# Performance work log

Measured on AMD Instinct MI355X. Metric: run time of the kernel, lower is better.

Reference implementation:

```python
import jax, jax.numpy as jnp
import numpy as np

N_HEAD = 32
N_KV_HEAD = 8
HEAD_DIM = 64
ROPE_THETA = 10000.0


def apply_rope(x):
    # x: [B, H, T, D], interleaved-pair RoPE (rotary_embedding_torch style)
    B, H, T, D = x.shape
    inv_freq = 1.0 / (ROPE_THETA ** (jnp.arange(0, D, 2, dtype=jnp.float32) / D))  # [D/2]
    ang = jnp.arange(T, dtype=jnp.float32)[:, None] * inv_freq[None, :]  # [T, D/2]
    cos = jnp.cos(ang)[None, None].astype(x.dtype)  # [1,1,T,D/2]
    sin = jnp.sin(ang)[None, None].astype(x.dtype)
    xe = x[..., 0::2]
    xo = x[..., 1::2]
    re = xe * cos - xo * sin
    ro = xo * cos + xe * sin
    return jnp.stack([re, ro], axis=-1).reshape(B, H, T, D)


def setup_inputs() -> dict:
    key = jax.random.key(0)
    ks = jax.random.split(key, 5)
    B, T, C = 2, 2048, 2048
    kv_dim = N_KV_HEAD * HEAD_DIM
    s = 0.02
    return {
        "x": jax.random.normal(ks[0], (B, T, C), jnp.float32),
        "wq": jax.random.normal(ks[1], (C, C), jnp.float32) * s,
        "wk": jax.random.normal(ks[2], (C, kv_dim), jnp.float32) * s,
        "wv": jax.random.normal(ks[3], (C, kv_dim), jnp.float32) * s,
        "wo": jax.random.normal(ks[4], (C, C), jnp.float32) * s,
    }


def reference(x, wq, wk, wv, wo):
    B, T, C = x.shape
    hd = HEAD_DIM
    q = (x @ wq).reshape(B, T, N_HEAD, hd).transpose(0, 2, 1, 3)      # [B,H,T,d]
    k = (x @ wk).reshape(B, T, N_KV_HEAD, hd).transpose(0, 2, 1, 3)   # [B,Hkv,T,d]
    v = (x @ wv).reshape(B, T, N_KV_HEAD, hd).transpose(0, 2, 1, 3)
    q = apply_rope(q)
    k = apply_rope(k)
    rep = N_HEAD // N_KV_HEAD
    k = jnp.repeat(k, rep, axis=1)  # repeat_interleave over head dim
    v = jnp.repeat(v, rep, axis=1)
    att = jnp.einsum('bhqd,bhkd->bhqk', q, k) * (1.0 / np.sqrt(hd))
    causal = jnp.tril(jnp.ones((T, T), dtype=bool))
    att = jnp.where(causal[None, None], att, jnp.finfo(att.dtype).min)
    att = jax.nn.softmax(att, axis=-1)
    y = jnp.einsum('bhqk,bhkd->bhqd', att, v)
    y = y.transpose(0, 2, 1, 3).reshape(B, T, C)
    return y @ wo
```

## Files before the change

kernel.cpp:

```cpp
#include <hip/hip_runtime.h>
#include <hip/hip_bf16.h>
#include <cstdint>
#include <cstddef>


using bf16 = __hip_bfloat16;
using f32x4  = __attribute__((ext_vector_type(4))) float;
using f32x16 = __attribute__((ext_vector_type(16))) float;
using short8 = __attribute__((ext_vector_type(8))) short;
using u32x4  = __attribute__((ext_vector_type(4))) unsigned int;

typedef __attribute__((address_space(1))) const void* gp1_t;
typedef __attribute__((address_space(3))) void*       lp3_t;

#define GLOAD_LDS16(g, l)                                                     \
  __builtin_amdgcn_global_load_lds((gp1_t)(const void*)(g), (lp3_t)(void*)(l), 16, 0, 0)

#define MFMA32(a, b, c) __builtin_amdgcn_mfma_f32_32x32x16_bf16(a, b, c, 0, 0, 0)

static constexpr int Bd  = 2;
static constexpr int Td  = 2048;
static constexpr int Cd  = 2048;
static constexpr int NH  = 32;
static constexpr int NKV = 8;
static constexpr int HD  = 64;
static constexpr int Md  = Bd * Td;

__device__ inline float bf2f(unsigned short u) {
  union { unsigned int i; float f; } v; v.i = ((unsigned int)u) << 16; return v.f;
}
__device__ inline unsigned short f2bfbits(float f) {
  union { float f; unsigned int u; } v; v.f = f;
  unsigned int r = v.u + 0x7fffu + ((v.u >> 16) & 1u);
  return (unsigned short)(r >> 16);
}
__device__ inline unsigned int pkbf(float a, float b) {
  unsigned int r;
  asm("v_cvt_pk_bf16_f32 %0, %1, %2" : "=v"(r) : "v"(a), "v"(b));
  return r;
}
__device__ inline void plswapf(float& a, float& b) {
  asm("v_permlane32_swap_b32 %0, %1" : "+v"(a), "+v"(b));
}
__device__ inline void plswapu(unsigned int& a, unsigned int& b) {
  asm("v_permlane32_swap_b32 %0, %1" : "+v"(a), "+v"(b));
}
__device__ inline float hmax16(const f32x16& v) {
  float a0 = fmaxf(v[0], v[1]),   a1 = fmaxf(v[2], v[3]);
  float a2 = fmaxf(v[4], v[5]),   a3 = fmaxf(v[6], v[7]);
  float a4 = fmaxf(v[8], v[9]),   a5 = fmaxf(v[10], v[11]);
  float a6 = fmaxf(v[12], v[13]), a7 = fmaxf(v[14], v[15]);
  float b0 = fmaxf(a0, a1), b1 = fmaxf(a2, a3);
  float b2 = fmaxf(a4, a5), b3 = fmaxf(a6, a7);
  return fmaxf(fmaxf(b0, b1), fmaxf(b2, b3));
}
__device__ inline float hsum16(const f32x16& v) {
  float a0 = v[0]+v[1],   a1 = v[2]+v[3],   a2 = v[4]+v[5],   a3 = v[6]+v[7];
  float a4 = v[8]+v[9],   a5 = v[10]+v[11], a6 = v[12]+v[13], a7 = v[14]+v[15];
  float b0 = a0+a1, b1 = a2+a3, b2 = a4+a5, b3 = a6+a7;
  return (b0+b1)+(b2+b3);
}

__global__ __launch_bounds__(256) void prep1_kernel(const float* __restrict__ x,
                                                    const float* __restrict__ wq,
                                                    const float* __restrict__ wk,
                                                    const float* __restrict__ wv,
                                                    bf16* __restrict__ xb,
                                                    bf16* __restrict__ w1) {
  __shared__ float tile[32][33];
  int bid = blockIdx.x, tid = threadIdx.x;
  if (bid < 8192) {
    int i = bid * 256 + tid;
    float4 v = ((const float4*)x)[i];
    ushort4 o;
    o.x = f2bfbits(v.x); o.y = f2bfbits(v.y); o.z = f2bfbits(v.z); o.w = f2bfbits(v.w);
    ((ushort4*)xb)[i] = o;
    return;
  }
  const float* in; bf16* out; int Cc, bx, by;
  if (bid < 12288)      { int l = bid - 8192;  in = wq; out = w1;                        Cc = 2048; bx = l & 63; by = l >> 6; }
  else if (bid < 13312) { int l = bid - 12288; in = wk; out = w1 + (size_t)2048 * 2048;  Cc = 512;  bx = l & 15; by = l >> 4; }
  else                  { int l = bid - 13312; in = wv; out = w1 + (size_t)2560 * 2048;  Cc = 512;  bx = l & 15; by = l >> 4; }
  int tx = tid & 31, ty = tid >> 5;
  int col = bx * 32 + tx;
#pragma unroll
  for (int i = 0; i < 4; ++i) {
    int row = by * 32 + ty + i * 8;
    tile[ty + i * 8][tx] = in[(size_t)row * Cc + col];
  }
  __syncthreads();
#pragma unroll
  for (int i = 0; i < 4; ++i) {
    int orow = bx * 32 + ty + i * 8;
    int ocol = by * 32 + tx;
    out[(size_t)orow * 2048 + ocol] = __float2bfloat16(tile[tx][ty + i * 8]);
  }
}

__global__ __launch_bounds__(256) void prep2_kernel(const float* __restrict__ wo,
                                                    bf16* __restrict__ w1,
                                                    bf16* __restrict__ Q,
                                                    bf16* __restrict__ K,
                                                    int qpairs, int total) {
  __shared__ float tile[32][33];
  int bid = blockIdx.x, tid = threadIdx.x;
  if (bid < 4096) {
    int bx = bid & 63, by = bid >> 6;
    int tx = tid & 31, ty = tid >> 5;
    int col = bx * 32 + tx;
#pragma unroll
    for (int i = 0; i < 4; ++i) {
      int row = by * 32 + ty + i * 8;
      tile[ty + i * 8][tx] = wo[(size_t)row * 2048 + col];
    }
    __syncthreads();
#pragma unroll
    for (int i = 0; i < 4; ++i) {
      int orow = bx * 32 + ty + i * 8;
      int ocol = by * 32 + tx;
      w1[(size_t)orow * 2048 + ocol] = __float2bfloat16(tile[tx][ty + i * 8]);
    }
    return;
  }
  int i = (bid - 4096) * 256 + tid;
  if (i >= total) return;
  unsigned int* buf; int p; float sc;
  if (i < qpairs) { buf = (unsigned int*)Q; p = i; sc = 0.18033688011112042f; }
  else            { buf = (unsigned int*)K; p = i - qpairs; sc = 1.0f; }
  int d2 = p & 31;
  int t  = (p >> 5) & (Td - 1);
  unsigned int packed = buf[p];
  float xe = bf2f((unsigned short)(packed & 0xffffu));
  float xo = bf2f((unsigned short)(packed >> 16));
  float inv = __builtin_amdgcn_exp2f((float)d2 * (-13.287712379549449f / 32.0f));
  float ang = (float)t * inv;
  float rev = ang * 0.15915494309189535f;
  rev = rev - floorf(rev);
  float s = __builtin_amdgcn_sinf(rev);
  float c = __builtin_amdgcn_cosf(rev);
  float re = (xe * c - xo * s) * sc;
  float ro = (xo * c + xe * s) * sc;
  buf[p] = (unsigned int)f2bfbits(re) | ((unsigned int)f2bfbits(ro) << 16);
}

template <int MODE>
__global__ __launch_bounds__(256) void gemm_bf16(const bf16* __restrict__ A,
                                                 const bf16* __restrict__ Bt,
                                                 void* __restrict__ Cp,
                                                 int M, int N, int K) {
  __shared__ __align__(16) bf16 Al[128 * 64];
  __shared__ __align__(16) bf16 Bl[128 * 64];
  int tid = threadIdx.x;
  int w = tid >> 6, lane = tid & 63;
  int lr = lane & 15, lg = lane >> 4;
  int m0 = blockIdx.x * 128, n0 = blockIdx.y * 128;
  int wr = w >> 1, wc = w & 1;
  f32x4 acc[4][4] = {};

  size_t Kb = (size_t)K * 2;
  int c8 = lane & 7, r8 = lane >> 3;
  const char* Asrc = (const char*)A + (size_t)(m0 + w * 8 + r8) * Kb + ((c8 ^ r8) << 4);
  const char* Bsrc = (const char*)Bt + (size_t)(n0 + w * 8 + r8) * Kb + ((c8 ^ r8) << 4);
  char* Ald = (char*)Al + w * 1024;
  char* Bld = (char*)Bl + w * 1024;

  for (int kt = 0; kt < K; kt += 64) {
#pragma unroll
    for (int j = 0; j < 4; ++j) {
      GLOAD_LDS16(Asrc + (size_t)j * 32 * Kb + (size_t)kt * 2, Ald + j * 4096);
      GLOAD_LDS16(Bsrc + (size_t)j * 32 * Kb + (size_t)kt * 2, Bld + j * 4096);
    }
    __syncthreads();
#pragma unroll
    for (int kk = 0; kk < 2; ++kk) {
      short8 af[4], bfr[4];
#pragma unroll
      for (int f = 0; f < 4; ++f) {
        int ra = wr * 64 + f * 16 + lr;
        int rb = wc * 64 + f * 16 + lr;
        int cb = (((kk << 2) | lg) ^ (lr & 7)) << 4;
        af[f]  = *(const short8*)((const char*)Al + (size_t)ra * 128 + cb);
        bfr[f] = *(const short8*)((const char*)Bl + (size_t)rb * 128 + cb);
      }
#pragma unroll
      for (int i = 0; i < 4; ++i)
#pragma unroll
        for (int j = 0; j < 4; ++j)
          acc[i][j] = __builtin_amdgcn_mfma_f32_16x16x32_bf16(af[i], bfr[j], acc[i][j], 0, 0, 0);
    }
    __syncthreads();
  }

  bf16* Qb  = (bf16*)Cp;
  bf16* Kb2 = Qb + (size_t)Bd * NH * Td * HD;
  bf16* Vtb = Kb2 + (size_t)Bd * NKV * Td * HD;

  if (MODE == 3 && n0 >= 2560) {
    int h  = (n0 - 2560 + wc * 64) >> 6;
    int b  = m0 >> 11;
    int tg = (m0 & 2047) + wr * 64;
    char* tb = (w < 2 ? (char*)Al : (char*)Bl) + (w & 1) * 8192;
#pragma unroll
    for (int i = 0; i < 4; ++i)
#pragma unroll
      for (int j = 0; j < 4; ++j)
#pragma unroll
        for (int r = 0; r < 4; r += 2) {
          int d  = j * 16 + lr;
          int tt = i * 16 + lg * 4 + r;
          unsigned int pk = pkbf(acc[i][j][r], acc[i][j][r + 1]);
          *(unsigned int*)(tb + (((size_t)d * 128 + tt * 2) ^ ((d & 7) << 4))) = pk;
        }
    asm volatile("s_waitcnt lgkmcnt(0)" ::: "memory");
    __builtin_amdgcn_sched_barrier(0);
    char* Vdst = (char*)Vtb + ((((size_t)b * NKV + h) * 64) * Td + tg) * 2;
#pragma unroll
    for (int p = 0; p < 8; ++p) {
      int d  = p * 8 + (lane >> 3);
      int tc = lane & 7;
      u32x4 v = *(const u32x4*)(tb + (((size_t)d * 128 + tc * 16) ^ ((d & 7) << 4)));
      *(u32x4*)(Vdst + (size_t)d * Td * 2 + tc * 16) = v;
    }
    return;
  }

#pragma unroll
  for (int i = 0; i < 4; ++i) {
#pragma unroll
    for (int j = 0; j < 4; ++j) {
#pragma unroll
      for (int r = 0; r < 4; ++r) {
        int mrow = m0 + wr * 64 + i * 16 + lg * 4 + r;
        int ncol = n0 + wc * 64 + j * 16 + lr;
        float v = acc[i][j][r];
        if (MODE == 2) {
          ((float*)Cp)[(size_t)mrow * N + ncol] = v;
        } else {
          int b = mrow >> 11, t = mrow & 2047;
          if (n0 < 2048) {
            int h = ncol >> 6, d = ncol & 63;
            Qb[(((size_t)b * NH + h) * Td + t) * HD + d] = __float2bfloat16(v);
          } else {
            int cc = ncol - 2048;
            int h = cc >> 6, d = cc & 63;
            Kb2[(((size_t)b * NKV + h) * Td + t) * HD + d] = __float2bfloat16(v);
          }
        }
      }
    }
  }
}

__global__ __launch_bounds__(512, 4) void attn_kernel(const bf16* __restrict__ Q,
                                                      const bf16* __restrict__ K,
                                                      const bf16* __restrict__ Vt,
                                                      bf16* __restrict__ Y) {
  __shared__ __align__(16) char lds[2 * 16384];
  int tid = threadIdx.x, w = tid >> 6, lane = tid & 63;
  int lq = lane & 31;
  int H  = lane >> 5;
  int qb = 7 - (int)blockIdx.y;
  int bh = blockIdx.x;
  int b = bh >> 5, h = bh & 31, kvh = h >> 2;
  int q0w = qb * 256 + w * 32;
  int qg  = q0w + lq;
  int tmax = qb * 4 + (w >> 1);
  int Nt   = qb * 4 + 4;

  const bf16* Qp = Q + (((size_t)b * NH + h) * Td) * HD;
  const char* Kg = (const char*)(K + (((size_t)b * NKV + kvh) * Td) * HD);
  const char* Vg = (const char*)(Vt + (((size_t)b * NKV + kvh) * HD) * Td);

  short8 qf[4];
#pragma unroll
  for (int ck = 0; ck < 4; ++ck)
    qf[ck] = *(const short8*)(Qp + (size_t)qg * HD + ck * 16 + H * 8);

  int srow   = lane >> 3;
  int scol16 = ((lane & 7) ^ srow) << 4;
  const char* Ksrc0 = Kg + (size_t)(w * 8 + srow) * 128 + scol16;
  const char* Vsrc0 = Vg + (size_t)(w * 8 + srow) * 4096 + scol16;
  char* KldsW[2] = { lds + w * 1024,          lds + 16384 + w * 1024 };
  char* VldsW[2] = { lds + 8192 + w * 1024,   lds + 24576 + w * 1024 };

#define STAGE_KV(tt, bb) do {                                                 \
    GLOAD_LDS16(Ksrc0 + (size_t)(tt) * 64 * 128, KldsW[bb]);                  \
    GLOAD_LDS16(Vsrc0 + (size_t)(tt) * 128,      VldsW[bb]);                  \
  } while (0)

  f32x16 acc0 = {}, acc1 = {};
  float m = -3e38f, l = 0.0f;
  int swz = (lq & 7) << 4;
  int rb0 = lq * 128, rb1 = (32 + lq) * 128;

  STAGE_KV(0, 0);
  asm volatile("s_waitcnt vmcnt(0)" ::: "memory");
  __syncthreads();

  for (int t = 0; t < Nt; ++t) {
    int cur = t & 1;
    if (t + 1 < Nt) STAGE_KV(t + 1, cur ^ 1);
    if (t <= tmax) {
      const char* Kl = lds + cur * 16384;
      const char* Vl = Kl + 8192;
      f32x16 s0 = {}, s1 = {};
      __builtin_amdgcn_s_setprio(1);
#pragma unroll
      for (int ck = 0; ck < 4; ++ck) {
        int c = (H * 16 + ck * 32) ^ swz;
        short8 kf0 = *(const short8*)(Kl + rb0 + c);
        short8 kf1 = *(const short8*)(Kl + rb1 + c);
        s0 = MFMA32(kf0, qf[ck], s0);
        s1 = MFMA32(kf1, qf[ck], s1);
      }
      __builtin_amdgcn_s_setprio(0);
      if (t == tmax) {
        int kvb = t * 64;
#pragma unroll
        for (int rr = 0; rr < 16; ++rr) {
          int krel = (rr & 3) + 8 * (rr >> 2) + 4 * H;
          if (kvb + krel > qg)      s0[rr] = -3e38f;
          if (kvb + 32 + krel > qg) s1[rr] = -3e38f;
        }
      }
      float mx = fmaxf(hmax16(s0), hmax16(s1));
      {
        float mb = mx;
        asm("" : "+v"(mb));
        plswapf(mx, mb);
        mx = fmaxf(mx, mb);
      }
      if (__any(mx > m + 8.0f)) {
        float mn = fmaxf(m, mx);
        float al = __builtin_amdgcn_exp2f(m - mn);
        m = mn;
        l *= al;
#pragma unroll
        for (int rr = 0; rr < 16; ++rr) { acc0[rr] *= al; acc1[rr] *= al; }
      }
#pragma unroll
      for (int rr = 0; rr < 16; ++rr) {
        s0[rr] = __builtin_amdgcn_exp2f(s0[rr] - m);
        s1[rr] = __builtin_amdgcn_exp2f(s1[rr] - m);
      }
      float ps = hsum16(s0) + hsum16(s1);
      {
        float pb = ps;
        asm("" : "+v"(pb));
        plswapf(ps, pb);
        ps += pb;
      }
      l += ps;
      short8 pf[4];
#pragma unroll
      for (int tt = 0; tt < 2; ++tt) {
        const f32x16& sv = tt ? s1 : s0;
#pragma unroll
        for (int a2 = 0; a2 < 2; ++a2) {
          unsigned int A0 = pkbf(sv[8*a2 + 0], sv[8*a2 + 1]);
          unsigned int A1 = pkbf(sv[8*a2 + 2], sv[8*a2 + 3]);
          unsigned int B0 = pkbf(sv[8*a2 + 4], sv[8*a2 + 5]);
          unsigned int B1 = pkbf(sv[8*a2 + 6], sv[8*a2 + 7]);
          plswapu(A0, B0);
          plswapu(A1, B1);
          u32x4 t4;
          t4[0] = A0; t4[1] = A1; t4[2] = B0; t4[3] = B1;
          pf[2*tt + a2] = __builtin_bit_cast(short8, t4);
        }
      }
      __builtin_amdgcn_s_setprio(1);
#pragma unroll
      for (int ks = 0; ks < 4; ++ks) {
        int c = (H * 16 + ks * 32) ^ swz;
        short8 vf0 = *(const short8*)(Vl + rb0 + c);
        short8 vf1 = *(const short8*)(Vl + rb1 + c);
        acc0 = MFMA32(vf0, pf[ks], acc0);
        acc1 = MFMA32(vf1, pf[ks], acc1);
      }
      __builtin_amdgcn_s_setprio(0);
    }
    asm volatile("s_waitcnt vmcnt(0)" ::: "memory");
    __syncthreads();
  }
#undef STAGE_KV

  float rn = 1.0f / l;
  bf16* Yp = Y + ((size_t)b * Td + qg) * Cd + h * HD;
#pragma unroll
  for (int rr = 0; rr < 16; rr += 2) {
    int d = (rr & 3) + 8 * (rr >> 2) + 4 * H;
    unsigned int w0 = pkbf(acc0[rr] * rn, acc0[rr + 1] * rn);
    unsigned int w1 = pkbf(acc1[rr] * rn, acc1[rr + 1] * rn);
    *(unsigned int*)(Yp + d)      = w0;
    *(unsigned int*)(Yp + 32 + d) = w1;
  }
}

extern "C" void kernel_launch(void* const* d_in, const int* in_sizes, int n_in,
                              void* d_out, int out_size, void* d_ws, size_t ws_size,
                              hipStream_t stream) {
  const float* x  = (const float*)d_in[0];
  const float* wq = (const float*)d_in[1];
  const float* wk = (const float*)d_in[2];
  const float* wv = (const float*)d_in[3];
  const float* wo = (const float*)d_in[4];

  char* ws = (char*)d_ws;
  const size_t o_xb = 0;
  const size_t o_w1 = o_xb + (size_t)Md * Cd * 2;
  const size_t o_Q  = o_w1 + (size_t)3072 * Cd * 2;
  const size_t o_K  = o_Q + (size_t)Bd * NH * Td * HD * 2;
  const size_t o_V  = o_K + (size_t)Bd * NKV * Td * HD * 2;

  bf16* xb  = (bf16*)(ws + o_xb);
  bf16* w1  = (bf16*)(ws + o_w1);
  bf16* Qb  = (bf16*)(ws + o_Q);
  bf16* Kb  = (bf16*)(ws + o_K);
  bf16* Vtb = (bf16*)(ws + o_V);
  bf16* yb  = xb;

  prep1_kernel<<<dim3(14336), dim3(256), 0, stream>>>(x, wq, wk, wv, xb, w1);
  gemm_bf16<3><<<dim3(Md / 128, 3072 / 128), dim3(256), 0, stream>>>(xb, w1, Qb, Md, 3072, Cd);
  {
    int qpairs = Bd * NH * Td * HD / 2;
    int kpairs = Bd * NKV * Td * HD / 2;
    int total = qpairs + kpairs;
    prep2_kernel<<<dim3(4096 + 20480), dim3(256), 0, stream>>>(wo, w1, Qb, Kb, qpairs, total);
  }
  attn_kernel<<<dim3(Bd * NH, 8), dim3(512), 0, stream>>>(Qb, Kb, Vtb, yb);
  gemm_bf16<2><<<dim3(Md / 128, Cd / 128), dim3(256), 0, stream>>>(yb, w1, d_out, Md, Cd, Cd);
}
```

Before: 216.3 us.

## Fuse RoPE into QKV GEMM epilogue and double-buffer GEMM LDS tiles

Moves the RoPE rotation and Q scaling out of the separate prep2 pass into the QKV GEMM epilogue. The pair partner comes from a lane shuffle, and sin/cos are computed per element. This removes a full read-modify-write pass over Q and K, and prep2 becomes a plain wo transpose kernel. The GEMM also gets double-buffered LDS staging so the next K tile loads while the current one computes, with launch bounds set for 2 blocks per CU. The epilogue now does more transcendental work per output element, and the doubled LDS may limit occupancy.

```diff
diff --git a/kernel.cpp b/kernel.cpp
--- a/kernel.cpp
+++ b/kernel.cpp
@@ -97,59 +97,34 @@
   }
 }
 
-__global__ __launch_bounds__(256) void prep2_kernel(const float* __restrict__ wo,
-                                                    bf16* __restrict__ w1,
-                                                    bf16* __restrict__ Q,
-                                                    bf16* __restrict__ K,
-                                                    int qpairs, int total) {
+__global__ __launch_bounds__(256) void transpose_f2b(const float* __restrict__ in,
+                                                     bf16* __restrict__ out,
+                                                     int R, int Cc) {
   __shared__ float tile[32][33];
-  int bid = blockIdx.x, tid = threadIdx.x;
-  if (bid < 4096) {
-    int bx = bid & 63, by = bid >> 6;
-    int tx = tid & 31, ty = tid >> 5;
-    int col = bx * 32 + tx;
-#pragma unroll
-    for (int i = 0; i < 4; ++i) {
-      int row = by * 32 + ty + i * 8;
-      tile[ty + i * 8][tx] = wo[(size_t)row * 2048 + col];
-    }
-    __syncthreads();
-#pragma unroll
-    for (int i = 0; i < 4; ++i) {
-      int orow = bx * 32 + ty + i * 8;
-      int ocol = by * 32 + tx;
-      w1[(size_t)orow * 2048 + ocol] = __float2bfloat16(tile[tx][ty + i * 8]);
-    }
-    return;
-  }
-  int i = (bid - 4096) * 256 + tid;
-  if (i >= total) return;
-  unsigned int* buf; int p; float sc;
-  if (i < qpairs) { buf = (unsigned int*)Q; p = i; sc = 0.18033688011112042f; }
-  else            { buf = (unsigned int*)K; p = i - qpairs; sc = 1.0f; }
-  int d2 = p & 31;
-  int t  = (p >> 5) & (Td - 1);
-  unsigned int packed = buf[p];
-  float xe = bf2f((unsigned short)(packed & 0xffffu));
-  float xo = bf2f((unsigned short)(packed >> 16));
-  float inv = __builtin_amdgcn_exp2f((float)d2 * (-13.287712379549449f / 32.0f));
-  float ang = (float)t * inv;
-  float rev = ang * 0.15915494309189535f;
-  rev = rev - floorf(rev);
-  float s = __builtin_amdgcn_sinf(rev);
-  float c = __builtin_amdgcn_cosf(rev);
-  float re = (xe * c - xo * s) * sc;
-  float ro = (xo * c + xe * s) * sc;
-  buf[p] = (unsigned int)f2bfbits(re) | ((unsigned int)f2bfbits(ro) << 16);
+  int tx = threadIdx.x & 31, ty = threadIdx.x >> 5;
+  int bx = blockIdx.x, by = blockIdx.y;
+  int col = bx * 32 + tx;
+#pragma unroll
+  for (int i = 0; i < 4; ++i) {
+    int row = by * 32 + ty + i * 8;
+    tile[ty + i * 8][tx] = in[(size_t)row * Cc + col];
+  }
+  __syncthreads();
+#pragma unroll
+  for (int i = 0; i < 4; ++i) {
+    int orow = bx * 32 + ty + i * 8;
+    int ocol = by * 32 + tx;
+    out[(size_t)orow * R + ocol] = __float2bfloat16(tile[tx][ty + i * 8]);
+  }
 }
 
 template <int MODE>
-__global__ __launch_bounds__(256) void gemm_bf16(const bf16* __restrict__ A,
-                                                 const bf16* __restrict__ Bt,
-                                                 void* __restrict__ Cp,
-                                                 int M, int N, int K) {
-  __shared__ __align__(16) bf16 Al[128 * 64];
-  __shared__ __align__(16) bf16 Bl[128 * 64];
+__global__ __launch_bounds__(256, 2) void gemm_bf16(const bf16* __restrict__ A,
+                                                    const bf16* __restrict__ Bt,
+                                                    void* __restrict__ Cp,
+                                                    int M, int N, int K) {
+  __shared__ __align__(16) bf16 Al[2][128 * 64];
+  __shared__ __align__(16) bf16 Bl[2][128 * 64];
   int tid = threadIdx.x;
   int w = tid >> 6, lane = tid & 63;
   int lr = lane & 15, lg = lane >> 4;
@@ -161,16 +136,26 @@
   int c8 = lane & 7, r8 = lane >> 3;
   const char* Asrc = (const char*)A + (size_t)(m0 + w * 8 + r8) * Kb + ((c8 ^ r8) << 4);
   const char* Bsrc = (const char*)Bt + (size_t)(n0 + w * 8 + r8) * Kb + ((c8 ^ r8) << 4);
-  char* Ald = (char*)Al + w * 1024;
-  char* Bld = (char*)Bl + w * 1024;
-
-  for (int kt = 0; kt < K; kt += 64) {
-#pragma unroll
-    for (int j = 0; j < 4; ++j) {
-      GLOAD_LDS16(Asrc + (size_t)j * 32 * Kb + (size_t)kt * 2, Ald + j * 4096);
-      GLOAD_LDS16(Bsrc + (size_t)j * 32 * Kb + (size_t)kt * 2, Bld + j * 4096);
-    }
-    __syncthreads();
+
+#define GSTAGE(kt, bb) do {                                                   \
+    char* ald = (char*)&Al[bb][0] + w * 1024;                                 \
+    char* bld = (char*)&Bl[bb][0] + w * 1024;                                 \
+    _Pragma("unroll")                                                         \
+    for (int j = 0; j < 4; ++j) {                                             \
+      GLOAD_LDS16(Asrc + (size_t)j * 32 * Kb + (size_t)(kt) * 2, ald + j * 4096); \
+      GLOAD_LDS16(Bsrc + (size_t)j * 32 * Kb + (size_t)(kt) * 2, bld + j * 4096); \
+    }                                                                         \
+  } while (0)
+
+  int nkt = K >> 6;
+  GSTAGE(0, 0);
+  __syncthreads();
+
+  for (int t = 0; t < nkt; ++t) {
+    int cur = t & 1;
+    if (t + 1 < nkt) GSTAGE((t + 1) << 6, cur ^ 1);
+    const char* Ab = (const char*)&Al[cur][0];
+    const char* Bb = (const char*)&Bl[cur][0];
 #pragma unroll
     for (int kk = 0; kk < 2; ++kk) {
       short8 af[4], bfr[4];
@@ -179,8 +164,8 @@
         int ra = wr * 64 + f * 16 + lr;
         int rb = wc * 64 + f * 16 + lr;
         int cb = (((kk << 2) | lg) ^ (lr & 7)) << 4;
-        af[f]  = *(const short8*)((const char*)Al + (size_t)ra * 128 + cb);
-        bfr[f] = *(const short8*)((const char*)Bl + (size_t)rb * 128 + cb);
+        af[f]  = *(const short8*)(Ab + (size_t)ra * 128 + cb);
+        bfr[f] = *(const short8*)(Bb + (size_t)rb * 128 + cb);
       }
 #pragma unroll
       for (int i = 0; i < 4; ++i)
@@ -190,6 +175,7 @@
     }
     __syncthreads();
   }
+#undef GSTAGE
 
   bf16* Qb  = (bf16*)Cp;
   bf16* Kb2 = Qb + (size_t)Bd * NH * Td * HD;
@@ -199,7 +185,7 @@
     int h  = (n0 - 2560 + wc * 64) >> 6;
     int b  = m0 >> 11;
     int tg = (m0 & 2047) + wr * 64;
-    char* tb = (w < 2 ? (char*)Al : (char*)Bl) + (w & 1) * 8192;
+    char* tb = (w < 2 ? (char*)&Al[0][0] : (char*)&Bl[0][0]) + (w & 1) * 8192;
 #pragma unroll
     for (int i = 0; i < 4; ++i)
 #pragma unroll
@@ -224,31 +210,53 @@
     return;
   }
 
-#pragma unroll
-  for (int i = 0; i < 4; ++i) {
+  if (MODE == 3) {
+    const float RC = -0.41524101186092029f;
+    float sc = (n0 < 2048) ? 0.18033688011112042f : 1.0f;
+    int odd = lane & 1;
 #pragma unroll
     for (int j = 0; j < 4; ++j) {
+      int ncol = n0 + wc * 64 + j * 16 + lr;
+      int d  = ncol & 63;
+      float inv = __builtin_amdgcn_exp2f((float)(d >> 1) * RC);
+#pragma unroll
+      for (int i = 0; i < 4; ++i) {
+#pragma unroll
+        for (int r = 0; r < 4; ++r) {
+          int mrow = m0 + wr * 64 + i * 16 + lg * 4 + r;
+          int t = mrow & 2047;
+          float v = acc[i][j][r];
+          float p = __shfl_xor(v, 1);
+          float rev = (float)t * inv * 0.15915494309189535f;
+          rev = rev - floorf(rev);
+          float s = __builtin_amdgcn_sinf(rev);
+          float c = __builtin_amdgcn_cosf(rev);
+          float res = odd ? (v * c + p * s) : (v * c - p * s);
+          res *= sc;
+          int b = mrow >> 11;
+          if (n0 < 2048) {
+            int h = ncol >> 6;
+            Qb[(((size_t)b * NH + h) * Td + t) * HD + d] = __float2bfloat16(res);
+          } else {
+            int h = (ncol - 2048) >> 6;
+            Kb2[(((size_t)b * NKV + h) * Td + t) * HD + d] = __float2bfloat16(res);
+          }
+        }
+      }
+    }
+    return;
+  }
+
+#pragma unroll
+  for (int i = 0; i < 4; ++i)
+#pragma unroll
+    for (int j = 0; j < 4; ++j)
 #pragma unroll
       for (int r = 0; r < 4; ++r) {
         int mrow = m0 + wr * 64 + i * 16 + lg * 4 + r;
         int ncol = n0 + wc * 64 + j * 16 + lr;
-        float v = acc[i][j][r];
-        if (MODE == 2) {
-          ((float*)Cp)[(size_t)mrow * N + ncol] = v;
-        } else {
-          int b = mrow >> 11, t = mrow & 2047;
-          if (n0 < 2048) {
-            int h = ncol >> 6, d = ncol & 63;
-            Qb[(((size_t)b * NH + h) * Td + t) * HD + d] = __float2bfloat16(v);
-          } else {
-            int cc = ncol - 2048;
-            int h = cc >> 6, d = cc & 63;
-            Kb2[(((size_t)b * NKV + h) * Td + t) * HD + d] = __float2bfloat16(v);
-          }
-        }
-      }
-    }
-  }
+        ((float*)Cp)[(size_t)mrow * N + ncol] = acc[i][j][r];
+      }
 }
 
 __global__ __launch_bounds__(512, 4) void attn_kernel(const bf16* __restrict__ Q,
@@ -421,12 +429,7 @@
 
   prep1_kernel<<<dim3(14336), dim3(256), 0, stream>>>(x, wq, wk, wv, xb, w1);
   gemm_bf16<3><<<dim3(Md / 128, 3072 / 128), dim3(256), 0, stream>>>(xb, w1, Qb, Md, 3072, Cd);
-  {
-    int qpairs = Bd * NH * Td * HD / 2;
-    int kpairs = Bd * NKV * Td * HD / 2;
-    int total = qpairs + kpairs;
-    prep2_kernel<<<dim3(4096 + 20480), dim3(256), 0, stream>>>(wo, w1, Qb, Kb, qpairs, total);
-  }
+  transpose_f2b<<<dim3(Cd / 32, Cd / 32), dim3(256), 0, stream>>>(wo, w1, Cd, Cd);
   attn_kernel<<<dim3(Bd * NH, 8), dim3(512), 0, stream>>>(Qb, Kb, Vtb, yb);
   gemm_bf16<2><<<dim3(Md / 128, Cd / 128), dim3(256), 0, stream>>>(yb, w1, d_out, Md, Cd, Cd);
 }
```

Measured after the change: 198.3 us. -8.3%, faster.
